# Kernel tuning notes

Hardware: AMD Instinct MI355X
Metric: run time of the kernel (lower is better)

The kernel has to match this reference:

```python
import jax, jax.numpy as jnp
import numpy as np

N_LAYERS = 2        # f_aux_layer_num
DIM = 512           # aux_dim
HEADS = 8           # aux_attn_num
HEAD = DIM // HEADS # 64 == aux_attn_dim
FFN_H = int(DIM * 2.0)  # ffn_factor = 2.0 -> 1024
BLOCK = 64          # f_block_size n
L_BLOCKS = 32
M = BLOCK + 1       # block + router token
EPS = 1e-5
THETA = 10000.0


def rms_norm(x, w):
    return x * jax.lax.rsqrt(jnp.mean(x * x, axis=-1, keepdims=True) + EPS) * w


def rotary(x):
    # x: [b, h, s, a]; matches RotaryEmb: halves rotated with outer(t, inv_freq)
    s, a = x.shape[2], x.shape[3]
    inv_freq = (1.0 / THETA) ** (jnp.arange(0, a, 2, dtype=jnp.float32) / a)
    freqs = jnp.arange(s, dtype=jnp.float32)[:, None] * inv_freq[None, :]  # [s, a/2]
    cos, sin = jnp.cos(freqs), jnp.sin(freqs)
    x1, x2 = jnp.split(x, 2, axis=-1)
    return jnp.concatenate([x1 * cos + x2 * sin, -x1 * sin + x2 * cos], axis=-1)


def setup_inputs() -> dict:
    key = jax.random.key(0)
    ks = jax.random.split(key, 10)
    B = 2
    S = L_BLOCKS * M
    x = jax.random.normal(ks[0], (B, L_BLOCKS * BLOCK, DIM), jnp.float32)
    doc = jnp.sort(jax.random.randint(ks[1], (B, S), 0, 4, dtype=jnp.int32), axis=-1)
    w = 0.02
    return {
        "x": x,
        "doc": doc,
        "router_token": jax.random.normal(ks[2], (DIM,), jnp.float32),
        "attn_w": jax.random.normal(ks[3], (N_LAYERS, DIM, 3 * DIM), jnp.float32) * w,
        "attn_o_w": jax.random.normal(ks[4], (N_LAYERS, DIM, DIM), jnp.float32) * w,
        "ffn_up_w": jax.random.normal(ks[5], (N_LAYERS, DIM, 2 * FFN_H), jnp.float32) * w,
        "ffn_down_w": jax.random.normal(ks[6], (N_LAYERS, FFN_H, DIM), jnp.float32) * w,
        "attn_norm_w": jnp.ones((N_LAYERS, DIM), jnp.float32),
        "ffn_norm_w": jnp.ones((N_LAYERS, DIM), jnp.float32),
    }


def reference(x, doc, router_token, attn_w, attn_o_w, ffn_up_w, ffn_down_w,
              attn_norm_w, ffn_norm_w):
    b = x.shape[0]
    # insert router token after each block: [b, l, n+1, d] -> [b, s, d]
    xb = x.reshape(b, L_BLOCKS, BLOCK, DIM)
    rt = jnp.broadcast_to(router_token, (b, L_BLOCKS, 1, DIM))
    h = jnp.concatenate([xb, rt], axis=2).reshape(b, L_BLOCKS * M, DIM)
    s = h.shape[1]

    # mask_mod_1: block-causal AND same-doc
    blk = jnp.arange(s) // M
    causal = blk[:, None] >= blk[None, :]                       # [s, s]
    mask = causal[None] & (doc[:, :, None] == doc[:, None, :])  # [b, s, s]
    neg = jnp.finfo(h.dtype).min
    scale = 1.0 / jnp.sqrt(jnp.float32(HEAD))

    def split_heads(t):
        return t.reshape(b, s, HEADS, HEAD).transpose(0, 2, 1, 3)

    for i in range(N_LAYERS):
        hn = rms_norm(h, attn_norm_w[i])
        qkv = hn @ attn_w[i]                       # [b, s, 3*dim]
        q, k, v = jnp.split(qkv, 3, axis=-1)
        q, k, v = split_heads(q), split_heads(k), split_heads(v)
        q, k = rotary(q), rotary(k)
        scores = jnp.einsum('bhqa,bhka->bhqk', q, k) * scale
        scores = jnp.where(mask[:, None], scores, neg)
        attn = jax.nn.softmax(scores, axis=-1)
        o = jnp.einsum('bhqk,bhka->bhqa', attn, v)
        o = o.transpose(0, 2, 1, 3).reshape(b, s, DIM)
        h = h + o @ attn_o_w[i]
        hf = rms_norm(h, ffn_norm_w[i])
        u1, u2 = jnp.split(hf @ ffn_up_w[i], 2, axis=-1)
        h = h + (jax.nn.silu(u1) * u2) @ ffn_down_w[i]

    # keep router-token slot of each block: [b, l, d]
    return h.reshape(b, L_BLOCKS, M, DIM)[:, :, -1]
```

## Files before the change

kernel.cpp:

```cpp
#include <hip/hip_runtime.h>
#include <math.h>

#define NB 2
#define LB 32
#define BLKN 64
#define MM 65
#define SS (LB*MM)
#define DD 512
#define NH 8
#define HD 64
#define FFH 1024
#define ROWS (NB*SS)
#define WT_LS 2621440

typedef __attribute__((ext_vector_type(8))) short bf16x8;
typedef __attribute__((ext_vector_type(4))) float f32x4;

__device__ __forceinline__ unsigned short f2bf(float f) {
    union { float f; unsigned u; } v; v.f = f;
    unsigned r = (v.u + 0x7FFFu + ((v.u >> 16) & 1u)) >> 16;
    return (unsigned short)r;
}
__device__ __forceinline__ float bf2f(unsigned short u) {
    union { unsigned u; float f; } v; v.u = ((unsigned)u) << 16; return v.f;
}

__device__ __forceinline__ void gload_lds16(const unsigned short* g, unsigned short* l) {
    __builtin_amdgcn_global_load_lds((const __attribute__((address_space(1))) unsigned int*)g,
                                     (__attribute__((address_space(3))) unsigned int*)l,
                                     16, 0, 0);
}

__device__ __forceinline__ int grow_map(int r) {
    return (r >> 5) * SS + (r & 31) * MM + BLKN;
}

template <int FIRST>
__global__ __launch_bounds__(256) void rms4_k(const unsigned short* __restrict__ hsrc,
                                              const float* __restrict__ x,
                                              const float* __restrict__ rt,
                                              const float* __restrict__ w,
                                              unsigned short* __restrict__ hout,
                                              unsigned short* __restrict__ out) {
    int row = blockIdx.x * 4 + (threadIdx.x >> 6);
    int lane = threadIdx.x & 63;
    float v[8];
    if (FIRST) {
        int s = row % SS, b = row / SS;
        int l = s / MM, j = s % MM;
        const float* sp = (j < BLKN) ? x + ((size_t)(b * LB + l) * BLKN + j) * DD : rt;
        float4 a = *(const float4*)(sp + lane * 8);
        float4 bq = *(const float4*)(sp + lane * 8 + 4);
        v[0] = a.x; v[1] = a.y; v[2] = a.z; v[3] = a.w;
        v[4] = bq.x; v[5] = bq.y; v[6] = bq.z; v[7] = bq.w;
    } else {
        bf16x8 h8 = *(const bf16x8*)(hsrc + (size_t)row * DD + lane * 8);
        #pragma unroll
        for (int j = 0; j < 8; ++j) v[j] = bf2f((unsigned short)h8[j]);
    }
    float ss = 0.0f;
    #pragma unroll
    for (int j = 0; j < 8; ++j) ss += v[j] * v[j];
    #pragma unroll
    for (int off = 32; off; off >>= 1) ss += __shfl_xor(ss, off);
    float r = rsqrtf(ss * (1.0f / 512.0f) + 1e-5f);
    float4 w0 = *(const float4*)(w + lane * 8);
    float4 w1 = *(const float4*)(w + lane * 8 + 4);
    float wv[8] = {w0.x, w0.y, w0.z, w0.w, w1.x, w1.y, w1.z, w1.w};
    unsigned short o8[8];
    #pragma unroll
    for (int j = 0; j < 8; ++j) o8[j] = f2bf(v[j] * r * wv[j]);
    *(bf16x8*)(out + (size_t)row * DD + lane * 8) = *(const bf16x8*)o8;
    if (FIRST) {
        unsigned short h8[8];
        #pragma unroll
        for (int j = 0; j < 8; ++j) h8[j] = f2bf(v[j]);
        *(bf16x8*)(hout + (size_t)row * DD + lane * 8) = *(const bf16x8*)h8;
    }
}

__global__ __launch_bounds__(256) void wtrans_all_k(const float* __restrict__ attn_w,
                                                    const float* __restrict__ attn_o_w,
                                                    const float* __restrict__ up_w,
                                                    const float* __restrict__ down_w,
                                                    unsigned short* __restrict__ wt) {
    __shared__ unsigned short T[64][66];
    int wg = blockIdx.x;
    int layer = wg >= 640;
    int r = wg - layer * 640;
    const float* W; int K, N; size_t dstOff; int perm = 0;
    if (r < 192)      { W = attn_w   + (size_t)layer * 512 * 1536; K = 512;  N = 1536; dstOff = 0; }
    else if (r < 256) { W = attn_o_w + (size_t)layer * 512 * 512;  K = 512;  N = 512;  dstOff = 786432;  r -= 192; }
    else if (r < 512) { W = up_w     + (size_t)layer * 512 * 2048; K = 512;  N = 2048; dstOff = 1048576; perm = 1; r -= 256; }
    else              { W = down_w   + (size_t)layer * 1024 * 512; K = 1024; N = 512;  dstOff = 2097152; r -= 512; }
    unsigned short* dst = wt + (size_t)layer * WT_LS + dstOff;
    int ntn = N >> 6;
    int n0 = (r % ntn) * 64, k0 = (r / ntn) * 64;
    int t = threadIdx.x;
    #pragma unroll
    for (int i = 0; i < 16; ++i) {
        int e = t + i * 256;
        int rr = e >> 6, cc = e & 63;
        T[rr][cc] = f2bf(W[(size_t)(k0 + rr) * N + n0 + cc]);
    }
    __syncthreads();
    #pragma unroll
    for (int i = 0; i < 16; ++i) {
        int e = t + i * 256;
        int rr = e >> 6, cc = e & 63;
        int n = n0 + rr;
        int nr = n;
        if (perm) {
            int p = n & 1023;
            nr = ((p >> 4) << 5) | ((n >> 10) << 4) | (p & 15);
        }
        dst[(size_t)nr * K + k0 + cc] = T[cc][rr];
    }
}

template <int ADD, int OBF, int ROPE, int SILU>
__global__ __launch_bounds__(256) void gemm128_k(const unsigned short* __restrict__ A,
                                                 const unsigned short* __restrict__ Wt,
                                                 void* __restrict__ Cp,
                                                 unsigned short* __restrict__ vT,
                                                 int K, int N, int colOff) {
    __shared__ unsigned short As[128 * 64];
    __shared__ unsigned short Bs[128 * 64];
    int t = threadIdx.x;
    int lane = t & 63, wv = t >> 6;
    int wm = wv >> 1, wn = wv & 1;
    int rowBase = blockIdx.y * 128, colBase = blockIdx.x * 128;
    int c = lane & 15, g = lane >> 4;
    int sw = (c & 7) << 4;

    f32x4 acc[4][4];
    #pragma unroll
    for (int mt = 0; mt < 4; ++mt)
        #pragma unroll
        for (int nt = 0; nt < 4; ++nt) { f32x4 z = {0, 0, 0, 0}; acc[mt][nt] = z; }

    for (int k0 = 0; k0 < K; k0 += 64) {
        __syncthreads();
        #pragma unroll
        for (int i = 0; i < 4; ++i) {
            int e0 = (i * 4 + wv) * 64;
            int e = e0 + lane;
            int row = e >> 3;
            int kb = ((e & 7) << 4) ^ ((row & 7) << 4);
            int gr = rowBase + row; if (gr > ROWS - 1) gr = ROWS - 1;
            gload_lds16(A + (size_t)gr * K + k0 + (kb >> 1), &As[e0 * 8]);
        }
        #pragma unroll
        for (int i = 0; i < 4; ++i) {
            int e0 = (i * 4 + wv) * 64;
            int e = e0 + lane;
            int row = e >> 3;
            int kb = ((e & 7) << 4) ^ ((row & 7) << 4);
            gload_lds16(Wt + (size_t)(colOff + colBase + row) * K + k0 + (kb >> 1), &Bs[e0 * 8]);
        }
        __syncthreads();

        bf16x8 af[4][2], bfr[4][2];
        #pragma unroll
        for (int mt = 0; mt < 4; ++mt)
            #pragma unroll
            for (int hf = 0; hf < 2; ++hf)
                af[mt][hf] = *(const bf16x8*)
                    &As[((wm * 64 + mt * 16 + c) * 128 + ((hf * 64 + g * 16) ^ sw)) >> 1];
        #pragma unroll
        for (int nt = 0; nt < 4; ++nt)
            #pragma unroll
            for (int hf = 0; hf < 2; ++hf)
                bfr[nt][hf] = *(const bf16x8*)
                    &Bs[((wn * 64 + nt * 16 + c) * 128 + ((hf * 64 + g * 16) ^ sw)) >> 1];
        __builtin_amdgcn_s_setprio(1);
        #pragma unroll
        for (int mt = 0; mt < 4; ++mt)
            #pragma unroll
            for (int nt = 0; nt < 4; ++nt) {
                acc[mt][nt] = __builtin_amdgcn_mfma_f32_16x16x32_bf16(af[mt][0], bfr[nt][0], acc[mt][nt], 0, 0, 0);
                acc[mt][nt] = __builtin_amdgcn_mfma_f32_16x16x32_bf16(af[mt][1], bfr[nt][1], acc[mt][nt], 0, 0, 0);
            }
        __builtin_amdgcn_s_setprio(0);
    }

    int sec = ROPE ? ((colOff + colBase + wn * 64) >> 9) : 0;
    if (ROPE && sec < 2) {
        #pragma unroll
        for (int mt = 0; mt < 4; ++mt)
            #pragma unroll
            for (int j = 0; j < 4; ++j) {
                int row = rowBase + wm * 64 + mt * 16 + g * 4 + j;
                int spos = row % SS;
                #pragma unroll
                for (int p = 0; p < 2; ++p) {
                    float jj = (float)(c + p * 16);
                    float inv = exp2f(jj * -0.41524101186092030f);
                    float fr = (float)spos * inv;
                    float sn, cs; __sincosf(fr, &sn, &cs);
                    float a = acc[mt][p][j], bb = acc[mt][p + 2][j];
                    acc[mt][p][j] = a * cs + bb * sn;
                    acc[mt][p + 2][j] = -a * sn + bb * cs;
                }
            }
    }

    #pragma unroll
    for (int mt = 0; mt < 4; ++mt)
        #pragma unroll
        for (int j = 0; j < 4; ++j) {
            int row = rowBase + wm * 64 + mt * 16 + g * 4 + j;
            if (row >= ROWS) continue;
            if (SILU) {
                unsigned short* gr = (unsigned short*)Cp + (size_t)row * 1024;
                #pragma unroll
                for (int ntp = 0; ntp < 2; ++ntp) {
                    int npr = colBase + wn * 64 + ntp * 32;
                    int p = ((npr >> 5) << 4) + c;
                    float u1 = acc[mt][2 * ntp][j];
                    float u2 = acc[mt][2 * ntp + 1][j];
                    gr[p] = f2bf((u1 / (1.0f + __expf(-u1))) * u2);
                }
            } else if (ROPE && sec == 2) {
                int bb = row / SS, s = row % SS;
                #pragma unroll
                for (int nt = 0; nt < 4; ++nt) {
                    int dg = colOff + colBase + wn * 64 + c + nt * 16 - 1024;
                    vT[(size_t)(bb * 512 + dg) * SS + s] = f2bf(acc[mt][nt][j]);
                }
            } else {
                size_t off = (size_t)row * N + colOff + colBase + wn * 64 + c;
                if (OBF) {
                    unsigned short* cr = (unsigned short*)Cp + off;
                    #pragma unroll
                    for (int nt = 0; nt < 4; ++nt) cr[nt * 16] = f2bf(acc[mt][nt][j]);
                } else {
                    float* cr = (float*)Cp + off;
                    #pragma unroll
                    for (int nt = 0; nt < 4; ++nt) {
                        if (ADD) cr[nt * 16] += acc[mt][nt][j];
                        else     cr[nt * 16] = acc[mt][nt][j];
                    }
                }
            }
        }
}

template <int MODE, int ADD>
__global__ __launch_bounds__(256) void gemm64_k(const unsigned short* __restrict__ A,
                                                const unsigned short* __restrict__ Wt,
                                                void* __restrict__ Cp,
                                                const unsigned short* __restrict__ Hsrc,
                                                float* __restrict__ outp,
                                                int K, int N) {
    __shared__ unsigned short As[64 * 64];
    __shared__ unsigned short Bs[128 * 64];
    int t = threadIdx.x;
    int lane = t & 63, wv = t >> 6;
    int wm = wv >> 1, wn = wv & 1;
    int rowBase = blockIdx.y * 64, colBase = blockIdx.x * 128;
    int c = lane & 15, g = lane >> 4;
    int sw = (c & 7) << 4;

    f32x4 acc[2][4];
    #pragma unroll
    for (int mt = 0; mt < 2; ++mt)
        #pragma unroll
        for (int nt = 0; nt < 4; ++nt) { f32x4 z = {0, 0, 0, 0}; acc[mt][nt] = z; }

    for (int k0 = 0; k0 < K; k0 += 64) {
        __syncthreads();
        #pragma unroll
        for (int i = 0; i < 2; ++i) {
            int e0 = (i * 4 + wv) * 64;
            int e = e0 + lane;
            int row = e >> 3;
            int kb = ((e & 7) << 4) ^ ((row & 7) << 4);
            int gr = rowBase + row;
            gload_lds16(A + (size_t)gr * K + k0 + (kb >> 1), &As[e0 * 8]);
        }
        #pragma unroll
        for (int i = 0; i < 4; ++i) {
            int e0 = (i * 4 + wv) * 64;
            int e = e0 + lane;
            int row = e >> 3;
            int kb = ((e & 7) << 4) ^ ((row & 7) << 4);
            gload_lds16(Wt + (size_t)(colBase + row) * K + k0 + (kb >> 1), &Bs[e0 * 8]);
        }
        __syncthreads();

        bf16x8 af[2][2], bfr[4][2];
        #pragma unroll
        for (int mt = 0; mt < 2; ++mt)
            #pragma unroll
            for (int hf = 0; hf < 2; ++hf)
                af[mt][hf] = *(const bf16x8*)
                    &As[((wm * 32 + mt * 16 + c) * 128 + ((hf * 64 + g * 16) ^ sw)) >> 1];
        #pragma unroll
        for (int nt = 0; nt < 4; ++nt)
            #pragma unroll
            for (int hf = 0; hf < 2; ++hf)
                bfr[nt][hf] = *(const bf16x8*)
                    &Bs[((wn * 64 + nt * 16 + c) * 128 + ((hf * 64 + g * 16) ^ sw)) >> 1];
        __builtin_amdgcn_s_setprio(1);
        #pragma unroll
        for (int mt = 0; mt < 2; ++mt)
            #pragma unroll
            for (int nt = 0; nt < 4; ++nt) {
                acc[mt][nt] = __builtin_amdgcn_mfma_f32_16x16x32_bf16(af[mt][0], bfr[nt][0], acc[mt][nt], 0, 0, 0);
                acc[mt][nt] = __builtin_amdgcn_mfma_f32_16x16x32_bf16(af[mt][1], bfr[nt][1], acc[mt][nt], 0, 0, 0);
            }
        __builtin_amdgcn_s_setprio(0);
    }

    #pragma unroll
    for (int mt = 0; mt < 2; ++mt)
        #pragma unroll
        for (int j = 0; j < 4; ++j) {
            int row = rowBase + wm * 32 + mt * 16 + g * 4 + j;
            int col = colBase + wn * 64 + c;
            if (MODE == 0) {
                if (ADD) {
                    unsigned short* cr = (unsigned short*)Cp + (size_t)row * N + col;
                    #pragma unroll
                    for (int nt = 0; nt < 4; ++nt)
                        cr[nt * 16] = f2bf(bf2f(cr[nt * 16]) + acc[mt][nt][j]);
                } else {
                    float* cr = (float*)Cp + (size_t)row * N + col;
                    #pragma unroll
                    for (int nt = 0; nt < 4; ++nt) cr[nt * 16] = acc[mt][nt][j];
                }
            } else if (MODE == 2) {
                int gr = grow_map(row);
                unsigned short* cr = (unsigned short*)Cp + (size_t)row * 512 + col;
                const unsigned short* hsr = Hsrc + (size_t)gr * 512 + col;
                #pragma unroll
                for (int nt = 0; nt < 4; ++nt)
                    cr[nt * 16] = f2bf(bf2f(hsr[nt * 16]) + acc[mt][nt][j]);
            } else if (MODE == 3) {
                float* cr = outp + (size_t)row * 512 + col;
                const unsigned short* hsr = Hsrc + (size_t)row * 512 + col;
                #pragma unroll
                for (int nt = 0; nt < 4; ++nt) cr[nt * 16] = bf2f(hsr[nt * 16]) + acc[mt][nt][j];
            } else {
                unsigned short* gr = (unsigned short*)Cp + (size_t)row * 1024;
                #pragma unroll
                for (int ntp = 0; ntp < 2; ++ntp) {
                    int npr = colBase + wn * 64 + ntp * 32;
                    int p = ((npr >> 5) << 4) + c;
                    float u1 = acc[mt][2 * ntp][j];
                    float u2 = acc[mt][2 * ntp + 1][j];
                    gr[p] = f2bf((u1 / (1.0f + __expf(-u1))) * u2);
                }
            }
        }
}

#define QR 80

__global__ __launch_bounds__(320) void attn_mfma_k(const unsigned short* __restrict__ qkv,
                                                   const unsigned short* __restrict__ vT,
                                                   const int* __restrict__ doc,
                                                   unsigned short* __restrict__ o) {
    __shared__ unsigned short QP[5760];
    __shared__ unsigned short Ks[2][64 * 64];
    __shared__ unsigned short Vs[2][64 * 64];
    __shared__ int docq[QR];
    __shared__ int dock[2][64];

    unsigned short* Qs = QP;
    unsigned short (*Ps)[16][72] = (unsigned short (*)[16][72])QP;

    int idx = blockIdx.x;
    int l = (idx < 256) ? (31 - (idx >> 4)) : ((idx - 256) >> 4);
    int b = (idx >> 3) & 1;
    int h = idx & 7;
    int t = threadIdx.x;
    int lane = t & 63;
    int wv = t >> 6;

    const unsigned short* qb = qkv + (size_t)b * SS * 1536;
    const unsigned short* vb = vT + (size_t)(b * 512 + h * 64) * SS;
    int rowq0 = l * MM;
    int kmax = (l + 1) * MM;

    #pragma unroll
    for (int it = 0; it < 2; ++it) {
        int ebase = it * 320 + wv * 64;
        int e = ebase + lane;
        int row = e >> 3;
        int kb = ((e & 7) << 4) ^ ((row & 7) << 4);
        int gr = rowq0 + row; if (gr > SS - 1) gr = SS - 1;
        gload_lds16(qb + (size_t)gr * 1536 + h * 64 + (kb >> 1), &Qs[ebase * 8]);
    }
    if (t < QR) docq[t] = (t < MM) ? doc[b * SS + rowq0 + t] : -999999;

    int d0 = doc[b * SS + rowq0];
    int lo = 0, hi = rowq0;
    while (lo < hi) {
        int mid = (lo + hi) >> 1;
        if (doc[b * SS + mid] < d0) lo = mid + 1; else hi = mid;
    }
    int kts = lo >> 6;
    int nkt = (kmax + 63) >> 6;

    const int mt = wv;
    const int g = lane >> 4;
    const int c = lane & 15;
    const int sw = (c & 7) << 4;

    auto stageK = [&](int kbase, int buf) {
        int ebase = wv * 64;
        int e = ebase + lane;
        int row = e >> 3;
        int kb = ((e & 7) << 4) ^ ((row & 7) << 4);
        int kg = kbase + row; if (kg > kmax - 1) kg = kmax - 1;
        gload_lds16(qb + (size_t)kg * 1536 + 512 + h * 64 + (kb >> 1), &Ks[buf][ebase * 8]);
        if (wv < 3) {
            int eb2 = 320 + wv * 64;
            int e2 = eb2 + lane;
            int row2 = e2 >> 3;
            int kb2 = ((e2 & 7) << 4) ^ ((row2 & 7) << 4);
            int kg2 = kbase + row2; if (kg2 > kmax - 1) kg2 = kmax - 1;
            gload_lds16(qb + (size_t)kg2 * 1536 + 512 + h * 64 + (kb2 >> 1), &Ks[buf][eb2 * 8]);
        }
    };
    auto stageV = [&](int kbase, int buf) {
        int ebase = wv * 64;
        int e = ebase + lane;
        int d = e >> 3;
        int kb = ((e & 7) << 4) ^ ((d & 7) << 4);
        gload_lds16(vb + (size_t)d * SS + kbase + (kb >> 1), &Vs[buf][ebase * 8]);
        if (wv < 3) {
            int eb2 = 320 + wv * 64;
            int e2 = eb2 + lane;
            int d2 = e2 >> 3;
            int kb2 = ((e2 & 7) << 4) ^ ((d2 & 7) << 4);
            gload_lds16(vb + (size_t)d2 * SS + kbase + (kb2 >> 1), &Vs[buf][eb2 * 8]);
        }
    };

    stageK(kts << 6, 0);
    stageV(kts << 6, 0);
    if (t < 64) {
        int kg = (kts << 6) + t;
        dock[0][t] = (kg < kmax) ? doc[b * SS + kg] : -1000000;
    }
    __syncthreads();

    bf16x8 aq[2];
    #pragma unroll
    for (int hf = 0; hf < 2; ++hf)
        aq[hf] = *(const bf16x8*)&Qs[((mt * 16 + c) * 128 + ((hf * 64 + g * 16) ^ sw)) >> 1];
    int dq[4];
    #pragma unroll
    for (int j = 0; j < 4; ++j) dq[j] = docq[mt * 16 + g * 4 + j];
    __syncthreads();

    f32x4 oacc[4];
    float m_[4], l_[4];
    #pragma unroll
    for (int nt = 0; nt < 4; ++nt) { f32x4 z = {0,0,0,0}; oacc[nt] = z; }
    #pragma unroll
    for (int j = 0; j < 4; ++j) { m_[j] = -1e30f; l_[j] = 0.0f; }

    for (int kt = kts; kt < nkt; ++kt) {
        int cur = (kt - kts) & 1;
        bool more = (kt + 1 < nkt);
        int dnx = 0;
        if (more) {
            stageK((kt + 1) << 6, cur ^ 1);
            stageV((kt + 1) << 6, cur ^ 1);
            if (t < 64) {
                int kg = ((kt + 1) << 6) + t;
                dnx = (kg < kmax) ? doc[b * SS + kg] : -1000000;
            }
        }

        f32x4 s[4];
        __builtin_amdgcn_s_setprio(1);
        #pragma unroll
        for (int sub = 0; sub < 4; ++sub) {
            f32x4 acc = {0, 0, 0, 0};
            #pragma unroll
            for (int hf = 0; hf < 2; ++hf) {
                bf16x8 bk = *(const bf16x8*)
                    &Ks[cur][((sub * 16 + c) * 128 + ((hf * 64 + g * 16) ^ sw)) >> 1];
                acc = __builtin_amdgcn_mfma_f32_16x16x32_bf16(aq[hf], bk, acc, 0, 0, 0);
            }
            s[sub] = acc;
        }
        __builtin_amdgcn_s_setprio(0);
        #pragma unroll
        for (int sub = 0; sub < 4; ++sub) {
            int dk = dock[cur][sub * 16 + c];
            #pragma unroll
            for (int j = 0; j < 4; ++j)
                s[sub][j] = (dq[j] == dk) ? s[sub][j] * 0.125f : -1e30f;
        }
        float mx[4];
        #pragma unroll
        for (int j = 0; j < 4; ++j)
            mx[j] = fmaxf(fmaxf(s[0][j], s[1][j]), fmaxf(s[2][j], s[3][j]));
        #pragma unroll
        for (int off = 1; off < 16; off <<= 1)
            #pragma unroll
            for (int j = 0; j < 4; ++j) mx[j] = fmaxf(mx[j], __shfl_xor(mx[j], off));
        float mn[4], sc[4], rs[4];
        #pragma unroll
        for (int j = 0; j < 4; ++j) {
            mn[j] = fmaxf(m_[j], mx[j]);
            sc[j] = __expf(m_[j] - mn[j]);
            m_[j] = mn[j];
            rs[j] = 0.0f;
        }
        #pragma unroll
        for (int sub = 0; sub < 4; ++sub)
            #pragma unroll
            for (int j = 0; j < 4; ++j) {
                float p = __expf(s[sub][j] - mn[j]);
                rs[j] += p;
                Ps[wv][g * 4 + j][sub * 16 + c] = f2bf(p);
            }
        #pragma unroll
        for (int off = 1; off < 16; off <<= 1)
            #pragma unroll
            for (int j = 0; j < 4; ++j) rs[j] += __shfl_xor(rs[j], off);
        #pragma unroll
        for (int j = 0; j < 4; ++j) l_[j] = l_[j] * sc[j] + rs[j];
        #pragma unroll
        for (int nt = 0; nt < 4; ++nt)
            #pragma unroll
            for (int j = 0; j < 4; ++j) oacc[nt][j] *= sc[j];
        __builtin_amdgcn_s_setprio(1);
        #pragma unroll
        for (int hf = 0; hf < 2; ++hf) {
            bf16x8 af = *(const bf16x8*)&Ps[wv][c][hf * 32 + g * 8];
            #pragma unroll
            for (int nt = 0; nt < 4; ++nt) {
                bf16x8 bv = *(const bf16x8*)
                    &Vs[cur][((nt * 16 + c) * 128 + ((hf * 64 + g * 16) ^ sw)) >> 1];
                oacc[nt] = __builtin_amdgcn_mfma_f32_16x16x32_bf16(af, bv, oacc[nt], 0, 0, 0);
            }
        }
        __builtin_amdgcn_s_setprio(0);

        if (more && t < 64) dock[cur ^ 1][t] = dnx;
        __syncthreads();
    }

    #pragma unroll
    for (int j = 0; j < 4; ++j) {
        int row = mt * 16 + g * 4 + j;
        if (row < MM) {
            float invl = 1.0f / l_[j];
            #pragma unroll
            for (int nt = 0; nt < 4; ++nt)
                o[(size_t)(b * SS + rowq0 + row) * DD + h * 64 + nt * 16 + c] =
                    f2bf(oacc[nt][j] * invl);
        }
    }
}

__global__ __launch_bounds__(256) void rattn_k(const unsigned short* __restrict__ hnb,
                                               const unsigned short* __restrict__ qkv,
                                               const unsigned short* __restrict__ vT,
                                               const unsigned short* __restrict__ wq,
                                               const int* __restrict__ doc,
                                               unsigned short* __restrict__ obr) {
    __shared__ float hn_r[DD];
    __shared__ float qs[HD];
    __shared__ float sc[SS];
    __shared__ float red_m[4], red_s[4];
    __shared__ float pacc[4][HD];

    int idx = blockIdx.x;
    int b = idx >> 8, h = (idx >> 5) & 7, l = idx & 31;
    int t = threadIdx.x;
    int lane = t & 63, wv = t >> 6;

    const unsigned short* qb = qkv + (size_t)b * SS * 1536;
    const unsigned short* vrow = vT + (size_t)(b * 512 + h * 64 + lane) * SS;
    int spos = l * MM + BLKN;
    int rowq = b * SS + spos;
    int kmax = (l + 1) * MM;

    {
        unsigned v = *(const unsigned*)(hnb + (size_t)rowq * DD + t * 2);
        hn_r[t * 2] = bf2f((unsigned short)(v & 0xffff));
        hn_r[t * 2 + 1] = bf2f((unsigned short)(v >> 16));
    }
    int dr = doc[rowq];
    int lo = 0, hi = spos;
    while (lo < hi) {
        int mid = (lo + hi) >> 1;
        if (doc[b * SS + mid] < dr) lo = mid + 1; else hi = mid;
    }
    __syncthreads();

    {
        float part = 0.0f;
        const unsigned short* wr = wq + (size_t)(h * 64 + lane) * DD + wv * 128;
        #pragma unroll
        for (int k8 = 0; k8 < 16; ++k8) {
            bf16x8 w8 = *(const bf16x8*)(wr + k8 * 8);
            #pragma unroll
            for (int j = 0; j < 8; ++j)
                part += hn_r[wv * 128 + k8 * 8 + j] * bf2f((unsigned short)w8[j]);
        }
        pacc[wv][lane] = part;
    }
    __syncthreads();
    if (wv == 0) {
        float dq = pacc[0][lane] + pacc[1][lane] + pacc[2][lane] + pacc[3][lane];
        float other = __shfl_xor(dq, 32);
        float jj = (float)(lane & 31);
        float inv = exp2f(jj * -0.41524101186092030f);
        float fr = (float)spos * inv;
        float sn, cs; __sincosf(fr, &sn, &cs);
        float q1 = (lane < 32) ? dq : other;
        float q2 = (lane < 32) ? other : dq;
        qs[lane] = (lane < 32) ? (q1 * cs + q2 * sn) : (-q1 * sn + q2 * cs);
    }
    __syncthreads();

    int dc = lane & 7, k8 = lane >> 3;
    float mx = -1e30f;
    for (int k0 = lo; k0 < kmax; k0 += 32) {
        int k = k0 + wv * 8 + k8;
        float d = 0.0f;
        if (k < kmax) {
            bf16x8 kv = *(const bf16x8*)(qb + (size_t)k * 1536 + 512 + h * 64 + dc * 8);
            #pragma unroll
            for (int j = 0; j < 8; ++j)
                d += bf2f((unsigned short)kv[j]) * qs[dc * 8 + j];
        }
        #pragma unroll
        for (int off = 1; off < 8; off <<= 1) d += __shfl_xor(d, off);
        if (k < kmax) {
            float s = d * 0.125f;
            if (dc == 0) sc[k] = s;
            mx = fmaxf(mx, s);
        }
    }
    #pragma unroll
    for (int off = 32; off; off >>= 1) mx = fmaxf(mx, __shfl_xor(mx, off));
    if (lane == 0) red_m[wv] = mx;
    __syncthreads();
    mx = fmaxf(fmaxf(red_m[0], red_m[1]), fmaxf(red_m[2], red_m[3]));

    float sum = 0.0f;
    for (int k = lo + t; k < kmax; k += 256) {
        float p = __expf(sc[k] - mx);
        sc[k] = p;
        sum += p;
    }
    #pragma unroll
    for (int off = 32; off; off >>= 1) sum += __shfl_xor(sum, off);
    if (lane == 0) red_s[wv] = sum;
    __syncthreads();
    sum = red_s[0] + red_s[1] + red_s[2] + red_s[3];

    float a0 = 0, a1 = 0, a2 = 0, a3 = 0;
    int k = lo + wv;
    for (; k + 12 < kmax; k += 16) {
        a0 += sc[k]      * bf2f(vrow[k]);
        a1 += sc[k + 4]  * bf2f(vrow[k + 4]);
        a2 += sc[k + 8]  * bf2f(vrow[k + 8]);
        a3 += sc[k + 12] * bf2f(vrow[k + 12]);
    }
    for (; k < kmax; k += 4)
        a0 += sc[k] * bf2f(vrow[k]);
    pacc[wv][lane] = (a0 + a1) + (a2 + a3);
    __syncthreads();
    if (wv == 0) {
        float o = (pacc[0][lane] + pacc[1][lane] + pacc[2][lane] + pacc[3][lane]) / sum;
        obr[(size_t)(b * LB + l) * DD + h * 64 + lane] = f2bf(o);
    }
}

extern "C" void kernel_launch(void* const* d_in, const int* in_sizes, int n_in,
                              void* d_out, int out_size, void* d_ws, size_t ws_size,
                              hipStream_t stream) {
    const float* x           = (const float*)d_in[0];
    const int*   doc         = (const int*)d_in[1];
    const float* rt          = (const float*)d_in[2];
    const float* attn_w      = (const float*)d_in[3];
    const float* attn_o_w    = (const float*)d_in[4];
    const float* ffn_up_w    = (const float*)d_in[5];
    const float* ffn_down_w  = (const float*)d_in[6];
    const float* attn_norm_w = (const float*)d_in[7];
    const float* ffn_norm_w  = (const float*)d_in[8];
    float* out = (float*)d_out;

    unsigned short* hb   = (unsigned short*)d_ws;
    unsigned short* qkvb = hb + (size_t)ROWS * 512;
    unsigned short* wt   = qkvb + (size_t)ROWS * 1536;
    unsigned short* hnb  = wt + (size_t)2 * WT_LS;
    unsigned short* ob   = hnb + (size_t)ROWS * 512;
    unsigned short* gb   = ob + (size_t)ROWS * 512;
    unsigned short* obr  = gb + (size_t)ROWS * 1024;
    unsigned short* hnr  = obr + 64 * 512;
    unsigned short* gbr  = hnr + 64 * 512;
    unsigned short* hr   = gbr + 64 * 1024;
    unsigned short* vTb  = hr + 64 * 512;

    wtrans_all_k<<<1280, 256, 0, stream>>>(attn_w, attn_o_w, ffn_up_w, ffn_down_w, wt);

    rms4_k<1><<<ROWS / 4, 256, 0, stream>>>(hb, x, rt, attn_norm_w, hb, hnb);
    gemm128_k<0, 1, 1, 0><<<dim3(12, 33), 256, 0, stream>>>(hnb, wt, qkvb, vTb, 512, 1536, 0);
    attn_mfma_k<<<512, 320, 0, stream>>>(qkvb, vTb, doc, ob);
    gemm64_k<0, 1><<<dim3(4, 65), 256, 0, stream>>>(ob, wt + 786432, hb, nullptr, nullptr, 512, 512);
    rms4_k<0><<<ROWS / 4, 256, 0, stream>>>(hb, x, rt, ffn_norm_w, nullptr, hnb);
    gemm128_k<0, 0, 0, 1><<<dim3(16, 33), 256, 0, stream>>>(hnb, wt + 1048576, gb, nullptr, 512, 2048, 0);
    gemm64_k<0, 1><<<dim3(4, 65), 256, 0, stream>>>(gb, wt + 2097152, hb, nullptr, nullptr, 1024, 512);

    unsigned short* wl = wt + (size_t)WT_LS;
    rms4_k<0><<<ROWS / 4, 256, 0, stream>>>(hb, x, rt, attn_norm_w + 512, nullptr, hnb);
    gemm128_k<0, 1, 1, 0><<<dim3(8, 33), 256, 0, stream>>>(hnb, wl, qkvb, vTb, 512, 1536, 512);
    rattn_k<<<512, 256, 0, stream>>>(hnb, qkvb, vTb, wl, doc, obr);
    gemm64_k<2, 0><<<dim3(4, 1), 256, 0, stream>>>(obr, wl + 786432, hr, hb, nullptr, 512, 512);
    rms4_k<0><<<16, 256, 0, stream>>>(hr, x, rt, ffn_norm_w + 512, nullptr, hnr);
    gemm64_k<4, 0><<<dim3(16, 1), 256, 0, stream>>>(hnr, wl + 1048576, gbr, nullptr, nullptr, 512, 2048);
    gemm64_k<3, 0><<<dim3(4, 1), 256, 0, stream>>>(gbr, wl + 2097152, nullptr, hr, out, 1024, 512);
}
```

Before: 215.4 us.

## Move V transpose out of QKV GEMM epilogue into a separate LDS-tiled kernel

The QKV GEMM epilogue no longer writes V transposed with scattered 2-byte stores. It writes V row-major, and a new kernel then transposes it into vT through shared memory with 16-byte loads and stores. For layer 2, the router attention reads V directly from the row-major qkv buffer, so the transpose is skipped there entirely. This trades uncoalesced strided epilogue stores for one extra launch plus a read and write of V, and rattn now does strided row reads of V.

```diff
diff --git a/kernel.cpp b/kernel.cpp
--- a/kernel.cpp
+++ b/kernel.cpp
@@ -118,11 +118,39 @@
     }
 }
 
+__global__ __launch_bounds__(256) void vtrans_k(const unsigned short* __restrict__ qkv,
+                                                unsigned short* __restrict__ vT) {
+    __shared__ unsigned short T[64][72];
+    int wg = blockIdx.x;
+    int st = wg % 33;
+    int dt = (wg / 33) % 8;
+    int b = wg / (33 * 8);
+    int s0 = st * 64, d0 = dt * 64;
+    int t = threadIdx.x;
+    #pragma unroll
+    for (int it = 0; it < 2; ++it) {
+        int r = (t >> 3) + it * 32;
+        int dd = (t & 7) * 8;
+        int s = s0 + r; if (s > SS - 1) s = SS - 1;
+        bf16x8 v8 = *(const bf16x8*)(qkv + ((size_t)(b * SS + s)) * 1536 + 1024 + d0 + dd);
+        #pragma unroll
+        for (int j = 0; j < 8; ++j) T[dd + j][r] = ((unsigned short*)&v8)[j];
+    }
+    __syncthreads();
+    #pragma unroll
+    for (int it = 0; it < 2; ++it) {
+        int d = (t >> 3) + it * 32;
+        int sc = (t & 7) * 8;
+        int s = s0 + sc;
+        if (s < SS)
+            *(bf16x8*)(vT + (size_t)(b * 512 + d0 + d) * SS + s) = *(const bf16x8*)&T[d][sc];
+    }
+}
+
 template <int ADD, int OBF, int ROPE, int SILU>
 __global__ __launch_bounds__(256) void gemm128_k(const unsigned short* __restrict__ A,
                                                  const unsigned short* __restrict__ Wt,
                                                  void* __restrict__ Cp,
-                                                 unsigned short* __restrict__ vT,
                                                  int K, int N, int colOff) {
     __shared__ unsigned short As[128 * 64];
     __shared__ unsigned short Bs[128 * 64];
@@ -184,25 +212,27 @@
         __builtin_amdgcn_s_setprio(0);
     }
 
-    int sec = ROPE ? ((colOff + colBase + wn * 64) >> 9) : 0;
-    if (ROPE && sec < 2) {
-        #pragma unroll
-        for (int mt = 0; mt < 4; ++mt)
-            #pragma unroll
-            for (int j = 0; j < 4; ++j) {
-                int row = rowBase + wm * 64 + mt * 16 + g * 4 + j;
-                int spos = row % SS;
+    if (ROPE) {
+        int sec = (colOff + colBase + wn * 64) >> 9;
+        if (sec < 2) {
+            #pragma unroll
+            for (int mt = 0; mt < 4; ++mt)
                 #pragma unroll
-                for (int p = 0; p < 2; ++p) {
-                    float jj = (float)(c + p * 16);
-                    float inv = exp2f(jj * -0.41524101186092030f);
-                    float fr = (float)spos * inv;
-                    float sn, cs; __sincosf(fr, &sn, &cs);
-                    float a = acc[mt][p][j], bb = acc[mt][p + 2][j];
-                    acc[mt][p][j] = a * cs + bb * sn;
-                    acc[mt][p + 2][j] = -a * sn + bb * cs;
+                for (int j = 0; j < 4; ++j) {
+                    int row = rowBase + wm * 64 + mt * 16 + g * 4 + j;
+                    int spos = row % SS;
+                    #pragma unroll
+                    for (int p = 0; p < 2; ++p) {
+                        float jj = (float)(c + p * 16);
+                        float inv = exp2f(jj * -0.41524101186092030f);
+                        float fr = (float)spos * inv;
+                        float sn, cs; __sincosf(fr, &sn, &cs);
+                        float a = acc[mt][p][j], bb = acc[mt][p + 2][j];
+                        acc[mt][p][j] = a * cs + bb * sn;
+                        acc[mt][p + 2][j] = -a * sn + bb * cs;
+                    }
                 }
-            }
+        }
     }
 
     #pragma unroll
@@ -220,13 +250,6 @@
                     float u1 = acc[mt][2 * ntp][j];
                     float u2 = acc[mt][2 * ntp + 1][j];
                     gr[p] = f2bf((u1 / (1.0f + __expf(-u1))) * u2);
-                }
-            } else if (ROPE && sec == 2) {
-                int bb = row / SS, s = row % SS;
-                #pragma unroll
-                for (int nt = 0; nt < 4; ++nt) {
-                    int dg = colOff + colBase + wn * 64 + c + nt * 16 - 1024;
-                    vT[(size_t)(bb * 512 + dg) * SS + s] = f2bf(acc[mt][nt][j]);
                 }
             } else {
                 size_t off = (size_t)row * N + colOff + colBase + wn * 64 + c;
@@ -564,7 +587,6 @@
 
 __global__ __launch_bounds__(256) void rattn_k(const unsigned short* __restrict__ hnb,
                                                const unsigned short* __restrict__ qkv,
-                                               const unsigned short* __restrict__ vT,
                                                const unsigned short* __restrict__ wq,
                                                const int* __restrict__ doc,
                                                unsigned short* __restrict__ obr) {
@@ -580,7 +602,6 @@
     int lane = t & 63, wv = t >> 6;
 
     const unsigned short* qb = qkv + (size_t)b * SS * 1536;
-    const unsigned short* vrow = vT + (size_t)(b * 512 + h * 64 + lane) * SS;
     int spos = l * MM + BLKN;
     int rowq = b * SS + spos;
     int kmax = (l + 1) * MM;
@@ -664,13 +685,13 @@
     float a0 = 0, a1 = 0, a2 = 0, a3 = 0;
     int k = lo + wv;
     for (; k + 12 < kmax; k += 16) {
-        a0 += sc[k]      * bf2f(vrow[k]);
-        a1 += sc[k + 4]  * bf2f(vrow[k + 4]);
-        a2 += sc[k + 8]  * bf2f(vrow[k + 8]);
-        a3 += sc[k + 12] * bf2f(vrow[k + 12]);
+        a0 += sc[k]      * bf2f(qb[(size_t)k * 1536 + 1024 + h * 64 + lane]);
+        a1 += sc[k + 4]  * bf2f(qb[(size_t)(k + 4) * 1536 + 1024 + h * 64 + lane]);
+        a2 += sc[k + 8]  * bf2f(qb[(size_t)(k + 8) * 1536 + 1024 + h * 64 + lane]);
+        a3 += sc[k + 12] * bf2f(qb[(size_t)(k + 12) * 1536 + 1024 + h * 64 + lane]);
     }
     for (; k < kmax; k += 4)
-        a0 += sc[k] * bf2f(vrow[k]);
+        a0 += sc[k] * bf2f(qb[(size_t)k * 1536 + 1024 + h * 64 + lane]);
     pacc[wv][lane] = (a0 + a1) + (a2 + a3);
     __syncthreads();
     if (wv == 0) {
@@ -708,17 +729,18 @@
     wtrans_all_k<<<1280, 256, 0, stream>>>(attn_w, attn_o_w, ffn_up_w, ffn_down_w, wt);
 
     rms4_k<1><<<ROWS / 4, 256, 0, stream>>>(hb, x, rt, attn_norm_w, hb, hnb);
-    gemm128_k<0, 1, 1, 0><<<dim3(12, 33), 256, 0, stream>>>(hnb, wt, qkvb, vTb, 512, 1536, 0);
+    gemm128_k<0, 1, 1, 0><<<dim3(12, 33), 256, 0, stream>>>(hnb, wt, qkvb, 512, 1536, 0);
+    vtrans_k<<<NB * 8 * 33, 256, 0, stream>>>(qkvb, vTb);
     attn_mfma_k<<<512, 320, 0, stream>>>(qkvb, vTb, doc, ob);
     gemm64_k<0, 1><<<dim3(4, 65), 256, 0, stream>>>(ob, wt + 786432, hb, nullptr, nullptr, 512, 512);
     rms4_k<0><<<ROWS / 4, 256, 0, stream>>>(hb, x, rt, ffn_norm_w, nullptr, hnb);
-    gemm128_k<0, 0, 0, 1><<<dim3(16, 33), 256, 0, stream>>>(hnb, wt + 1048576, gb, nullptr, 512, 2048, 0);
+    gemm128_k<0, 0, 0, 1><<<dim3(16, 33), 256, 0, stream>>>(hnb, wt + 1048576, gb, 512, 2048, 0);
     gemm64_k<0, 1><<<dim3(4, 65), 256, 0, stream>>>(gb, wt + 2097152, hb, nullptr, nullptr, 1024, 512);
 
     unsigned short* wl = wt + (size_t)WT_LS;
     rms4_k<0><<<ROWS / 4, 256, 0, stream>>>(hb, x, rt, attn_norm_w + 512, nullptr, hnb);
-    gemm128_k<0, 1, 1, 0><<<dim3(8, 33), 256, 0, stream>>>(hnb, wl, qkvb, vTb, 512, 1536, 512);
-    rattn_k<<<512, 256, 0, stream>>>(hnb, qkvb, vTb, wl, doc, obr);
+    gemm128_k<0, 1, 1, 0><<<dim3(8, 33), 256, 0, stream>>>(hnb, wl, qkvb, 512, 1536, 512);
+    rattn_k<<<512, 256, 0, stream>>>(hnb, qkvb, wl, doc, obr);
     gemm64_k<2, 0><<<dim3(4, 1), 256, 0, stream>>>(obr, wl + 786432, hr, hb, nullptr, 512, 512);
     rms4_k<0><<<16, 256, 0, stream>>>(hr, x, rt, ffn_norm_w + 512, nullptr, hnr);
     gemm64_k<4, 0><<<dim3(16, 1), 256, 0, stream>>>(hnr, wl + 1048576, gbr, nullptr, nullptr, 512, 2048);
```

Measured after the change: 188.2 us. -12.6%, faster.
